# Optimization experiments

Hardware: AMD Instinct MI355X
Metric: run time of the kernel (lower is better)

Reference implementation:

```python
import jax, jax.numpy as jnp
import numpy as np
import math

B, T, H, W = 32, 256, 16, 16
NE, NH, NL = 768, 12, 8
DH = NE // NH
SEQ_LEN = 1024


def _ln(x, g, b, eps=1e-5):
    m = jnp.mean(x, axis=-1, keepdims=True)
    v = jnp.mean((x - m) ** 2, axis=-1, keepdims=True)
    return (x - m) * jax.lax.rsqrt(v + eps) * g + b


def setup_inputs() -> dict:
    key = jax.random.key(0)
    ks = jax.random.split(key, 24)
    s = 0.02
    d = {}
    d["img_feat"] = jax.random.normal(ks[0], (B, 2048, H, W), jnp.float32)
    d["vm_patches"] = jax.random.normal(ks[1], (B, T, 256), jnp.float32)
    d["fm_patches"] = jax.random.normal(ks[2], (B, T, 256), jnp.float32)
    # token embedding params
    d["conv_w"] = jax.random.normal(ks[3], (NE // 2, 2048, 3, 3), jnp.float32) * s
    d["conv_b"] = jnp.zeros((NE // 2,), jnp.float32)
    d["vm_w"] = jax.random.normal(ks[4], (256, NE // 4), jnp.float32) * s
    d["vm_b"] = jnp.zeros((NE // 4,), jnp.float32)
    d["fm_w"] = jax.random.normal(ks[5], (256, NE // 4), jnp.float32) * s
    d["fm_b"] = jnp.zeros((NE // 4,), jnp.float32)
    d["pos_emb"] = jax.random.normal(ks[6], (SEQ_LEN, NE), jnp.float32) * s
    # stacked per-layer block params (leading dim NL, consumed by lax.scan)
    d["ln1_g"] = jnp.ones((NL, NE), jnp.float32)
    d["ln1_b"] = jnp.zeros((NL, NE), jnp.float32)
    d["Wq"] = jax.random.normal(ks[7], (NL, NE, NE), jnp.float32) * s
    d["bq"] = jnp.zeros((NL, NE), jnp.float32)
    d["Wk"] = jax.random.normal(ks[8], (NL, NE, NE), jnp.float32) * s
    d["bk"] = jnp.zeros((NL, NE), jnp.float32)
    d["Wv"] = jax.random.normal(ks[9], (NL, NE, NE), jnp.float32) * s
    d["bv"] = jnp.zeros((NL, NE), jnp.float32)
    d["Wo"] = jax.random.normal(ks[10], (NL, NE, NE), jnp.float32) * s
    d["bo"] = jnp.zeros((NL, NE), jnp.float32)
    d["ln2_g"] = jnp.ones((NL, NE), jnp.float32)
    d["ln2_b"] = jnp.zeros((NL, NE), jnp.float32)
    d["W1"] = jax.random.normal(ks[11], (NL, NE, 4 * NE), jnp.float32) * s
    d["b1"] = jnp.zeros((NL, 4 * NE), jnp.float32)
    d["W2"] = jax.random.normal(ks[12], (NL, 4 * NE, NE), jnp.float32) * s
    d["b2"] = jnp.zeros((NL, NE), jnp.float32)
    # prediction head params
    d["dec_ln1_g"] = jnp.ones((NE,), jnp.float32)
    d["dec_ln1_b"] = jnp.zeros((NE,), jnp.float32)
    d["dec_w"] = jax.random.normal(ks[13], (NE, NE), jnp.float32) * s
    d["dec_b"] = jnp.zeros((NE,), jnp.float32)
    d["dec_ln2_g"] = jnp.ones((NE,), jnp.float32)
    d["dec_ln2_b"] = jnp.zeros((NE,), jnp.float32)
    d["head_w"] = jax.random.normal(ks[14], (NE, 256), jnp.float32) * s
    d["head_b"] = jnp.zeros((256,), jnp.float32)
    return d


def reference(img_feat, vm_patches, fm_patches, conv_w, conv_b, vm_w, vm_b, fm_w, fm_b,
              pos_emb, ln1_g, ln1_b, Wq, bq, Wk, bk, Wv, bv, Wo, bo, ln2_g, ln2_b,
              W1, b1, W2, b2, dec_ln1_g, dec_ln1_b, dec_w, dec_b, dec_ln2_g, dec_ln2_b,
              head_w, head_b):
    # conv token embed: [B,2048,H,W] -> [B, NE//2, H, W] -> [B, T, NE//2]
    i_emb = jax.lax.conv_general_dilated(
        img_feat, conv_w, (1, 1), "SAME",
        dimension_numbers=("NCHW", "OIHW", "NCHW")) + conv_b[None, :, None, None]
    i_emb = i_emb.reshape(B, NE // 2, T).transpose(0, 2, 1)
    vm_emb = vm_patches @ vm_w + vm_b  # [B,T,NE//4]
    fm_emb = fm_patches @ fm_w + fm_b  # [B,T,NE//4]
    x = jnp.concatenate([i_emb, vm_emb, fm_emb], axis=2) + pos_emb[:T][None]  # [B,T,NE]

    scale = 1.0 / math.sqrt(DH)

    def block(x, p):
        g1, bb1_, wq, bq_, wk, bk_, wv, bv_, wo, bo_, g2, bb2_, w1, bm1, w2, bm2 = p
        h = _ln(x, g1, bb1_)
        q = (h @ wq + bq_).reshape(B, T, NH, DH)
        k = (h @ wk + bk_).reshape(B, T, NH, DH)
        v = (h @ wv + bv_).reshape(B, T, NH, DH)
        # mask in the original forward is hard-coded all-ones -> no masking
        att = jax.nn.softmax(jnp.einsum('bthd,bshd->bhts', q, k) * scale, axis=-1)
        y = jnp.einsum('bhts,bshd->bthd', att, v).reshape(B, T, NE)
        x = x + y @ wo + bo_
        h2 = _ln(x, g2, bb2_)
        x = x + jax.nn.gelu(h2 @ w1 + bm1, approximate=False) @ w2 + bm2
        return x, None

    x, _ = jax.lax.scan(block, x, (ln1_g, ln1_b, Wq, bq, Wk, bk, Wv, bv, Wo, bo,
                                   ln2_g, ln2_b, W1, b1, W2, b2))

    # Transformer_Prediction head
    x = _ln(x, dec_ln1_g, dec_ln1_b)
    x = jax.nn.gelu(x @ dec_w + dec_b, approximate=False)
    x = _ln(x, dec_ln2_g, dec_ln2_b)
    return x @ head_w + head_b  # [B,T,256]
```

## Files before the change

### kernel.cpp

```cpp
#include <hip/hip_runtime.h>
#include <stdint.h>

typedef short short8 __attribute__((ext_vector_type(8)));
typedef float v4f __attribute__((ext_vector_type(4)));

#define EPI_BF16    0
#define EPI_GELU    1
#define EPI_XPOS    3
#define EPI_ATOM    5
#define EPI_ATOMOUT 6

__device__ __forceinline__ uint16_t f2bf(float f) {
  uint32_t u = __float_as_uint(f);
  u += 0x7fffu + ((u >> 16) & 1u);
  return (uint16_t)(u >> 16);
}
__device__ __forceinline__ float bf2f(uint16_t h) {
  return __uint_as_float(((uint32_t)h) << 16);
}
__device__ __forceinline__ float gelu_f(float v) {
  return 0.5f * v * (1.f + erff(v * 0.70710678118654752f));
}
__device__ __forceinline__ void gld16(const uint16_t* g, uint16_t* l) {
  __builtin_amdgcn_global_load_lds(
      (const __attribute__((address_space(1))) void*)g,
      (__attribute__((address_space(3))) void*)l, 16, 0, 0);
}

struct TDesc {
  const float* src;
  uint16_t* dst;
  int K, N, batch;
  long long sstride, dstride;
  int tilesK, tilesN;
  long long tileStart;
};
struct TTable {
  TDesc d[12];
  int nd;
  long long totalTiles;
};

__global__ __launch_bounds__(256) void transpose_convert_kernel(TTable tt) {
  __shared__ float tile[32][33];
  const int tid = threadIdx.x;
  for (long long t = blockIdx.x; t < tt.totalTiles; t += gridDim.x) {
    int di = 0;
    while (di + 1 < tt.nd && t >= tt.d[di + 1].tileStart) di++;
    const TDesc d = tt.d[di];
    long long loc = t - d.tileStart;
    int perB = d.tilesK * d.tilesN;
    int bi = (int)(loc / perB);
    int r = (int)(loc % perB);
    int tk = r / d.tilesN, tn = r % d.tilesN;
    const float* src = d.src + (long long)bi * d.sstride;
    uint16_t* dst = d.dst + (long long)bi * d.dstride;
    int k0 = tk * 32, n0 = tn * 32;
#pragma unroll
    for (int p = 0; p < 4; p++) {
      int i = (tid >> 5) + p * 8;
      int k = k0 + i, n = n0 + (tid & 31);
      float v = 0.f;
      if (k < d.K && n < d.N) v = src[(long long)k * d.N + n];
      tile[i][tid & 31] = v;
    }
    __syncthreads();
#pragma unroll
    for (int p = 0; p < 4; p++) {
      int i = (tid >> 5) + p * 8;
      int n = n0 + i, k = k0 + (tid & 31);
      if (n < d.N && k < d.K) dst[(long long)n * d.K + k] = f2bf(tile[tid & 31][i]);
    }
    __syncthreads();
  }
}

__global__ __launch_bounds__(256) void conv_w_transpose(const float* __restrict__ src,
                                                        uint16_t* __restrict__ dst) {
  __shared__ float lds[2304];
  const int n = blockIdx.y;
  const int c0 = blockIdx.x * 256;
  const float* s = src + (size_t)n * 18432 + (size_t)c0 * 9;
  for (int j = threadIdx.x; j < 2304; j += 256) lds[j] = s[j];
  __syncthreads();
#pragma unroll
  for (int tap = 0; tap < 9; tap++)
    dst[(size_t)n * 18432 + tap * 2048 + c0 + threadIdx.x] =
        f2bf(lds[threadIdx.x * 9 + tap]);
}

__global__ __launch_bounds__(256) void img_pad_kernel(const float* __restrict__ img,
                                                      uint16_t* __restrict__ imgp) {
  __shared__ float tile[64][65];
  const int tid = threadIdx.x;
  const int b = blockIdx.z, ict = blockIdx.y, xyt = blockIdx.x;
  const int ic0 = ict * 64, xy0 = xyt * 64;
  const float* src = img + ((size_t)b * 2048 + ic0) * 256 + xy0;
#pragma unroll
  for (int p = 0; p < 16; p++) {
    int i = (tid >> 6) + p * 4;
    int j = tid & 63;
    tile[i][j] = src[(size_t)i * 256 + j];
  }
  __syncthreads();
#pragma unroll
  for (int p = 0; p < 16; p++) {
    int j = (tid >> 6) + p * 4;
    int i = tid & 63;
    int xy = xy0 + j;
    int y = xy >> 4, x = xy & 15;
    imgp[(((size_t)b * 18 + y + 1) * 18 + (x + 1)) * 2048 + ic0 + i] = f2bf(tile[i][j]);
  }
}

__global__ __launch_bounds__(256) void prep_kernel(const float* __restrict__ bq,
                                                   const float* __restrict__ bk,
                                                   const float* __restrict__ bv,
                                                   float* __restrict__ bqkv,
                                                   const float* __restrict__ vm,
                                                   const float* __restrict__ fm,
                                                   uint16_t* __restrict__ vmb,
                                                   uint16_t* __restrict__ fmb) {
  int idx = blockIdx.x * 256 + threadIdx.x;
  if (idx < 2097152) {
    vmb[idx] = f2bf(vm[idx]);
    fmb[idx] = f2bf(fm[idx]);
  }
  if (idx < 18432) {
    int l = idx / 2304, c = idx % 2304;
    float v = (c < 768) ? bq[l * 768 + c]
                        : ((c < 1536) ? bk[l * 768 + c - 768] : bv[l * 768 + c - 1536]);
    bqkv[idx] = v;
  }
}

__global__ __launch_bounds__(256) void xinit_kernel(const float* __restrict__ convb,
                                                    const float* __restrict__ pos,
                                                    float* __restrict__ x) {
  int idx = blockIdx.x * 256 + threadIdx.x;
  if (idx >= 8192 * 384) return;
  int m = idx / 384, n = idx % 384;
  x[(size_t)m * 768 + n] = convb[n] + pos[(size_t)(m & 255) * 768 + n];
}

template <int BF16IN>
__global__ __launch_bounds__(256) void ln_kernel(const void* __restrict__ inv,
                                                 const float* __restrict__ g,
                                                 const float* __restrict__ bta,
                                                 uint16_t* __restrict__ out) {
  const int row = blockIdx.x;
  const int tid = threadIdx.x;
  const float* inf = (const float*)inv;
  const uint16_t* inb = (const uint16_t*)inv;
  const size_t base = (size_t)row * 768;
  float v[3];
#pragma unroll
  for (int i = 0; i < 3; i++) {
    int c = tid + i * 256;
    v[i] = BF16IN ? bf2f(inb[base + c]) : inf[base + c];
  }
  float s = v[0] + v[1] + v[2];
  float s2 = v[0] * v[0] + v[1] * v[1] + v[2] * v[2];
#pragma unroll
  for (int d = 1; d < 64; d <<= 1) {
    s += __shfl_xor(s, d, 64);
    s2 += __shfl_xor(s2, d, 64);
  }
  __shared__ float ps[4], ps2[4];
  int wave = tid >> 6, lane = tid & 63;
  if (lane == 0) { ps[wave] = s; ps2[wave] = s2; }
  __syncthreads();
  s = ps[0] + ps[1] + ps[2] + ps[3];
  s2 = ps2[0] + ps2[1] + ps2[2] + ps2[3];
  float mean = s * (1.f / 768.f);
  float var = s2 * (1.f / 768.f) - mean * mean;
  float rs = rsqrtf(var + 1e-5f);
#pragma unroll
  for (int i = 0; i < 3; i++) {
    int c = tid + i * 256;
    out[base + c] = f2bf((v[i] - mean) * rs * g[c] + bta[c]);
  }
}

template <int AMODE, int EPI>
__global__ __launch_bounds__(256, 4) void gemm_kernel(
    const uint16_t* __restrict__ A, const uint16_t* __restrict__ Bt,
    const float* __restrict__ bias, int N, int K,
    float* xout,
    const float* __restrict__ pos, int colOff,
    uint16_t* __restrict__ outb, float* __restrict__ outf, int ldc) {
  __shared__ uint16_t ldsA[8192];
  __shared__ uint16_t ldsB[4096];
  const int tid = threadIdx.x;
  const int lane = tid & 63, wave = tid >> 6;
  const int l15 = lane & 15, q8 = (lane >> 4) << 3;
  const int row0 = blockIdx.x * 128, col0 = blockIdx.y * 64;
  const int kPer = K / (int)gridDim.z;
  const int kbeg = kPer * (int)blockIdx.z;
  const int wm = wave & 1, wn = wave >> 1;

  const uint16_t* srcP[6];
  uint16_t* dstP[6];
  bool isA[6];
#pragma unroll
  for (int c = 0; c < 6; c++) {
    int j = wave * 6 + c;
    if (j < 16) {
      int mt8 = j >> 1, ks = j & 1;
      int m = row0 + mt8 * 16 + l15;
      const uint16_t* s;
      if (AMODE == 0) {
        s = A + (size_t)m * K + ks * 32 + q8;
      } else {
        int b_ = m >> 8, y_ = (m >> 4) & 15, x_ = m & 15;
        s = A + ((size_t)((b_ * 18 + y_) * 18 + x_)) * 2048 + ks * 32 + q8;
      }
      srcP[c] = s;
      dstP[c] = &ldsA[j * 512];
      isA[c] = true;
    } else {
      int fb = j - 16;
      int nt = fb >> 1, ks = fb & 1;
      int n = col0 + nt * 16 + l15;
      srcP[c] = Bt + (size_t)n * K + ks * 32 + q8;
      dstP[c] = &ldsB[fb * 512];
      isA[c] = false;
    }
  }

  v4f acc[4][2];
#pragma unroll
  for (int i = 0; i < 4; i++)
#pragma unroll
    for (int j = 0; j < 2; j++) acc[i][j] = (v4f){0.f, 0.f, 0.f, 0.f};

  for (int k0 = kbeg; k0 < kbeg + kPer; k0 += 64) {
    size_t ao;
    if (AMODE == 1) {
      int kq = k0 >> 11;
      int ky = (kq >= 6) ? 2 : ((kq >= 3) ? 1 : 0);
      int kx = kq - ky * 3;
      ao = (size_t)((ky * 18 + kx) * 2048) + (size_t)(k0 & 2047);
    } else {
      ao = (size_t)k0;
    }
    __syncthreads();
#pragma unroll
    for (int c = 0; c < 6; c++) {
      size_t offs = (AMODE == 1) ? (isA[c] ? ao : (size_t)k0) : (size_t)k0;
      gld16(srcP[c] + offs, dstP[c]);
    }
    __syncthreads();
#pragma unroll
    for (int ks = 0; ks < 2; ks++) {
      short8 af[4], bfr[2];
#pragma unroll
      for (int mt = 0; mt < 4; mt++)
        af[mt] = *(const short8*)&ldsA[(((wm * 4 + mt) * 2) + ks) * 512 + lane * 8];
#pragma unroll
      for (int nt = 0; nt < 2; nt++)
        bfr[nt] = *(const short8*)&ldsB[(((wn * 2 + nt) * 2) + ks) * 512 + lane * 8];
#pragma unroll
      for (int mt = 0; mt < 4; mt++)
#pragma unroll
        for (int nt = 0; nt < 2; nt++)
          acc[mt][nt] =
              __builtin_amdgcn_mfma_f32_16x16x32_bf16(af[mt], bfr[nt], acc[mt][nt], 0, 0, 0);
    }
  }

#pragma unroll
  for (int mt = 0; mt < 4; mt++) {
    int mbase = row0 + wm * 64 + mt * 16 + ((lane >> 4) << 2);
#pragma unroll
    for (int nt = 0; nt < 2; nt++) {
      int n = col0 + wn * 32 + nt * 16 + l15;
      float bv;
      if (EPI == EPI_ATOM)
        bv = (bias != nullptr && blockIdx.z == 0) ? bias[n] : 0.f;
      else if (EPI == EPI_ATOMOUT)
        bv = (blockIdx.z == 0) ? bias[n] : 0.f;
      else
        bv = bias[n];
      v4f a = acc[mt][nt];
#pragma unroll
      for (int r = 0; r < 4; r++) {
        int m = mbase + r;
        float v = a[r] + bv;
        if (EPI == EPI_BF16) {
          outb[(size_t)m * ldc + n] = f2bf(v);
        } else if (EPI == EPI_GELU) {
          outb[(size_t)m * ldc + n] = f2bf(gelu_f(v));
        } else if (EPI == EPI_XPOS) {
          xout[(size_t)m * 768 + colOff + n] = v + pos[(size_t)(m & 255) * 768 + colOff + n];
        } else if (EPI == EPI_ATOM) {
          atomicAdd(&xout[(size_t)m * 768 + colOff + n], v);
        } else if (EPI == EPI_ATOMOUT) {
          atomicAdd(&outf[(size_t)m * ldc + n], v);
        }
      }
    }
  }
}

template <int AMODE, int EPI>
__global__ __launch_bounds__(256, 2) void gemm128_kernel(
    const uint16_t* __restrict__ A, const uint16_t* __restrict__ Bt,
    const float* __restrict__ bias, int N, int K,
    float* xout,
    const float* __restrict__ pos, int colOff,
    uint16_t* __restrict__ outb, float* __restrict__ outf, int ldc) {
  __shared__ uint16_t lds[2][16384];
  const int tid = threadIdx.x;
  const int lane = tid & 63, wave = tid >> 6;
  const int l15 = lane & 15, q8 = (lane >> 4) << 3;
  const int row0 = blockIdx.x * 128, col0 = blockIdx.y * 128;
  const int kPer = K / (int)gridDim.z;
  const int kbeg = kPer * (int)blockIdx.z;
  const int nt = kPer >> 6;
  const int wm = wave & 1, wn = wave >> 1;

  const uint16_t* srcP[8];
  int off[8];
  bool isAv[8];
#pragma unroll
  for (int c = 0; c < 8; c++) {
    int j = wave * 8 + c;
    if (j < 16) {
      int mt8 = j >> 1, ks = j & 1;
      int m = row0 + mt8 * 16 + l15;
      const uint16_t* s;
      if (AMODE == 0) {
        s = A + (size_t)m * K + ks * 32 + q8;
      } else {
        int b_ = m >> 8, y_ = (m >> 4) & 15, x_ = m & 15;
        s = A + ((size_t)((b_ * 18 + y_) * 18 + x_)) * 2048 + ks * 32 + q8;
      }
      srcP[c] = s;
      off[c] = j * 512;
      isAv[c] = true;
    } else {
      int fb = j - 16;
      int nt16 = fb >> 1, ks = fb & 1;
      int n = col0 + nt16 * 16 + l15;
      srcP[c] = Bt + (size_t)n * K + ks * 32 + q8;
      off[c] = 8192 + fb * 512;
      isAv[c] = false;
    }
  }

  auto STAGE = [&](int t) {
    int k0 = kbeg + t * 64;
    size_t aoB = (size_t)k0, aoA;
    if (AMODE == 1) {
      int kq = k0 >> 11;
      int ky = (kq >= 6) ? 2 : ((kq >= 3) ? 1 : 0);
      int kx = kq - ky * 3;
      aoA = (size_t)((ky * 18 + kx) * 2048) + (size_t)(k0 & 2047);
    } else {
      aoA = aoB;
    }
    uint16_t* lb = &lds[t & 1][0];
#pragma unroll
    for (int c = 0; c < 8; c++) gld16(srcP[c] + (isAv[c] ? aoA : aoB), lb + off[c]);
  };

  v4f acc[4][4];
#pragma unroll
  for (int i = 0; i < 4; i++)
#pragma unroll
    for (int j = 0; j < 4; j++) acc[i][j] = (v4f){0.f, 0.f, 0.f, 0.f};

  STAGE(0);
  if (nt > 1) STAGE(1);

  for (int t = 0; t < nt; t++) {
    if (t + 1 < nt)
      asm volatile("s_waitcnt vmcnt(8)" ::: "memory");
    else
      asm volatile("s_waitcnt vmcnt(0)" ::: "memory");
    __builtin_amdgcn_s_barrier();

    const uint16_t* lb = &lds[t & 1][0];
#pragma unroll
    for (int ks = 0; ks < 2; ks++) {
      short8 af[4], bfr[4];
#pragma unroll
      for (int mt = 0; mt < 4; mt++)
        af[mt] = *(const short8*)&lb[(((wm * 4 + mt) * 2) + ks) * 512 + lane * 8];
#pragma unroll
      for (int nt2 = 0; nt2 < 4; nt2++)
        bfr[nt2] = *(const short8*)&lb[8192 + (((wn * 4 + nt2) * 2) + ks) * 512 + lane * 8];
#pragma unroll
      for (int mt = 0; mt < 4; mt++)
#pragma unroll
        for (int nt2 = 0; nt2 < 4; nt2++)
          acc[mt][nt2] =
              __builtin_amdgcn_mfma_f32_16x16x32_bf16(af[mt], bfr[nt2], acc[mt][nt2], 0, 0, 0);
    }

    __builtin_amdgcn_s_barrier();
    if (t + 2 < nt) STAGE(t + 2);
  }

#pragma unroll
  for (int mt = 0; mt < 4; mt++) {
    int mbase = row0 + wm * 64 + mt * 16 + ((lane >> 4) << 2);
#pragma unroll
    for (int nt2 = 0; nt2 < 4; nt2++) {
      int n = col0 + wn * 64 + nt2 * 16 + l15;
      float bv;
      if (EPI == EPI_ATOM)
        bv = (bias != nullptr && blockIdx.z == 0) ? bias[n] : 0.f;
      else if (EPI == EPI_ATOMOUT)
        bv = (blockIdx.z == 0) ? bias[n] : 0.f;
      else
        bv = bias[n];
      v4f a = acc[mt][nt2];
#pragma unroll
      for (int r = 0; r < 4; r++) {
        int m = mbase + r;
        float v = a[r] + bv;
        if (EPI == EPI_BF16) {
          outb[(size_t)m * ldc + n] = f2bf(v);
        } else if (EPI == EPI_GELU) {
          outb[(size_t)m * ldc + n] = f2bf(gelu_f(v));
        } else if (EPI == EPI_XPOS) {
          xout[(size_t)m * 768 + colOff + n] = v + pos[(size_t)(m & 255) * 768 + colOff + n];
        } else if (EPI == EPI_ATOM) {
          atomicAdd(&xout[(size_t)m * 768 + colOff + n], v);
        } else if (EPI == EPI_ATOMOUT) {
          atomicAdd(&outf[(size_t)m * ldc + n], v);
        }
      }
    }
  }
}

__global__ __launch_bounds__(256) void attn_kernel(const uint16_t* __restrict__ qkv,
                                                   uint16_t* __restrict__ y) {
  __shared__ uint16_t KP[18432];
  __shared__ uint16_t Vt[64 * 264];
  uint16_t* Kl = KP;
  uint16_t(*Pl)[16 * 264] = (uint16_t(*)[16 * 264])KP;
  const int tid = threadIdx.x, lane = tid & 63, wave = tid >> 6;
  const int qc = blockIdx.x, h = blockIdx.y, b = blockIdx.z;
  const uint16_t* base = qkv + (size_t)b * 256 * 2304;
  const uint16_t* kb = base + 768 + h * 64;
  const uint16_t* vb = base + 1536 + h * 64;

#pragma unroll
  for (int i = 0; i < 8; i++) {
    int c = i * 256 + tid;
    int t = c >> 3, dh = (c & 7) * 8;
    uint4 d = *(const uint4*)(kb + (size_t)t * 2304 + dh);
    *(uint4*)&Kl[t * 72 + dh] = d;
  }
#pragma unroll
  for (int i = 0; i < 8; i++) {
    int c = i * 256 + tid;
    int t = c >> 3, dh = (c & 7) * 8;
    uint4 d = *(const uint4*)(vb + (size_t)t * 2304 + dh);
    const uint16_t* e = (const uint16_t*)&d;
#pragma unroll
    for (int j = 0; j < 8; j++) Vt[(dh + j) * 264 + t] = e[j];
  }
  __syncthreads();

  const int t0 = qc * 64 + wave * 16;
  const uint16_t* qb = base + h * 64;
  const int l15 = lane & 15, q4 = (lane >> 4) << 3;
  short8 aq0 = *(const short8*)(qb + (size_t)(t0 + l15) * 2304 + q4);
  short8 aq1 = *(const short8*)(qb + (size_t)(t0 + l15) * 2304 + 32 + q4);

  v4f s[16];
#pragma unroll
  for (int jt = 0; jt < 16; jt++) {
    short8 b0 = *(const short8*)&Kl[(jt * 16 + l15) * 72 + q4];
    short8 b1 = *(const short8*)&Kl[(jt * 16 + l15) * 72 + 32 + q4];
    v4f z = (v4f){0.f, 0.f, 0.f, 0.f};
    z = __builtin_amdgcn_mfma_f32_16x16x32_bf16(aq0, b0, z, 0, 0, 0);
    s[jt] = __builtin_amdgcn_mfma_f32_16x16x32_bf16(aq1, b1, z, 0, 0, 0);
  }

  float mx[4], sm[4];
#pragma unroll
  for (int r = 0; r < 4; r++) mx[r] = -1e30f;
#pragma unroll
  for (int jt = 0; jt < 16; jt++)
#pragma unroll
    for (int r = 0; r < 4; r++) {
      float v = s[jt][r] * 0.125f;
      s[jt][r] = v;
      mx[r] = fmaxf(mx[r], v);
    }
#pragma unroll
  for (int r = 0; r < 4; r++) {
#pragma unroll
    for (int d = 1; d < 16; d <<= 1) mx[r] = fmaxf(mx[r], __shfl_xor(mx[r], d, 64));
    sm[r] = 0.f;
  }
#pragma unroll
  for (int jt = 0; jt < 16; jt++)
#pragma unroll
    for (int r = 0; r < 4; r++) {
      float e = __expf(s[jt][r] - mx[r]);
      s[jt][r] = e;
      sm[r] += e;
    }
#pragma unroll
  for (int r = 0; r < 4; r++) {
#pragma unroll
    for (int d = 1; d < 16; d <<= 1) sm[r] += __shfl_xor(sm[r], d, 64);
    sm[r] = 1.f / sm[r];
  }

  __syncthreads();

  const int rbase = (lane >> 4) << 2;
#pragma unroll
  for (int jt = 0; jt < 16; jt++)
#pragma unroll
    for (int r = 0; r < 4; r++)
      Pl[wave][(rbase + r) * 264 + jt * 16 + l15] = f2bf(s[jt][r] * sm[r]);
  __syncthreads();

  v4f o[4];
#pragma unroll
  for (int nt = 0; nt < 4; nt++) o[nt] = (v4f){0.f, 0.f, 0.f, 0.f};
#pragma unroll
  for (int ks = 0; ks < 8; ks++) {
    short8 ap = *(const short8*)&Pl[wave][l15 * 264 + ks * 32 + q4];
#pragma unroll
    for (int nt = 0; nt < 4; nt++) {
      short8 bv8 = *(const short8*)&Vt[(nt * 16 + l15) * 264 + ks * 32 + q4];
      o[nt] = __builtin_amdgcn_mfma_f32_16x16x32_bf16(ap, bv8, o[nt], 0, 0, 0);
    }
  }
#pragma unroll
  for (int nt = 0; nt < 4; nt++)
#pragma unroll
    for (int r = 0; r < 4; r++)
      y[(size_t)(b * 256 + t0 + rbase + r) * 768 + h * 64 + nt * 16 + l15] = f2bf(o[nt][r]);
}

extern "C" void kernel_launch(void* const* d_in, const int* in_sizes, int n_in,
                              void* d_out, int out_size, void* d_ws, size_t ws_size,
                              hipStream_t stream) {
  const float* img   = (const float*)d_in[0];
  const float* vmp   = (const float*)d_in[1];
  const float* fmp   = (const float*)d_in[2];
  const float* convw = (const float*)d_in[3];
  const float* convb = (const float*)d_in[4];
  const float* vmw   = (const float*)d_in[5];
  const float* vmb_  = (const float*)d_in[6];
  const float* fmw   = (const float*)d_in[7];
  const float* fmb_  = (const float*)d_in[8];
  const float* pos   = (const float*)d_in[9];
  const float* ln1g  = (const float*)d_in[10];
  const float* ln1b  = (const float*)d_in[11];
  const float* Wq    = (const float*)d_in[12];
  const float* bq    = (const float*)d_in[13];
  const float* Wk    = (const float*)d_in[14];
  const float* bk    = (const float*)d_in[15];
  const float* Wv    = (const float*)d_in[16];
  const float* bv    = (const float*)d_in[17];
  const float* Wo    = (const float*)d_in[18];
  const float* bo    = (const float*)d_in[19];
  const float* ln2g  = (const float*)d_in[20];
  const float* ln2b  = (const float*)d_in[21];
  const float* W1    = (const float*)d_in[22];
  const float* b1    = (const float*)d_in[23];
  const float* W2    = (const float*)d_in[24];
  const float* b2    = (const float*)d_in[25];
  const float* dln1g = (const float*)d_in[26];
  const float* dln1b = (const float*)d_in[27];
  const float* decw  = (const float*)d_in[28];
  const float* decb  = (const float*)d_in[29];
  const float* dln2g = (const float*)d_in[30];
  const float* dln2b = (const float*)d_in[31];
  const float* headw = (const float*)d_in[32];
  const float* headb = (const float*)d_in[33];
  float* out = (float*)d_out;

  char* wsb = (char*)d_ws;
  size_t off = 0;
  auto alloc = [&](size_t nbytes) -> void* {
    off = (off + 255) & ~(size_t)255;
    void* p = wsb + off;
    off += nbytes;
    return p;
  };
  uint16_t* WtQKV  = (uint16_t*)alloc(8ull * 2304 * 768 * 2);
  uint16_t* WtO    = (uint16_t*)alloc(8ull * 768 * 768 * 2);
  uint16_t* Wt1    = (uint16_t*)alloc(8ull * 3072 * 768 * 2);
  uint16_t* Wt2    = (uint16_t*)alloc(8ull * 768 * 3072 * 2);
  uint16_t* WtConv = (uint16_t*)alloc(384ull * 9 * 2048 * 2);
  uint16_t* WtVm   = (uint16_t*)alloc(192ull * 256 * 2);
  uint16_t* WtFm   = (uint16_t*)alloc(192ull * 256 * 2);
  uint16_t* WtDec  = (uint16_t*)alloc(768ull * 768 * 2);
  uint16_t* WtHead = (uint16_t*)alloc(256ull * 768 * 2);
  uint16_t* imgp   = (uint16_t*)alloc(32ull * 18 * 18 * 2048 * 2);
  uint16_t* vmb    = (uint16_t*)alloc(8192ull * 256 * 2);
  uint16_t* fmb    = (uint16_t*)alloc(8192ull * 256 * 2);
  float*    bqkv   = (float*)alloc(8ull * 2304 * 4);
  float*    x      = (float*)alloc(8192ull * 768 * 4);
  uint16_t* hbuf   = (uint16_t*)alloc(8192ull * 768 * 2);
  uint16_t* qkvb   = (uint16_t*)alloc(8192ull * 2304 * 2);
  uint16_t* ybuf   = (uint16_t*)alloc(8192ull * 768 * 2);
  uint16_t* ubuf   = (uint16_t*)alloc(8192ull * 3072 * 2);
  uint16_t* u2buf  = (uint16_t*)alloc(8192ull * 768 * 2);
  if (off > ws_size) return;

  hipMemsetAsync(imgp, 0, 32ull * 18 * 18 * 2048 * 2, stream);
  hipMemsetAsync(out, 0, (size_t)out_size * 4, stream);

  TTable tt;
  int nd = 0;
  long long tiles = 0;
  auto addT = [&](const float* src, uint16_t* dst, int K, int N, int batch,
                  long long sstr, long long dstr) {
    TDesc& d = tt.d[nd];
    d.src = src; d.dst = dst; d.K = K; d.N = N; d.batch = batch;
    d.sstride = sstr; d.dstride = dstr;
    d.tilesK = (K + 31) / 32; d.tilesN = (N + 31) / 32;
    d.tileStart = tiles;
    tiles += (long long)d.tilesK * d.tilesN * batch;
    nd++;
  };
  addT(Wq, WtQKV,           768, 768, 8, 589824, 1769472);
  addT(Wk, WtQKV + 589824,  768, 768, 8, 589824, 1769472);
  addT(Wv, WtQKV + 1179648, 768, 768, 8, 589824, 1769472);
  addT(Wo, WtO,             768, 768, 8, 589824, 589824);
  addT(W1, Wt1,             768, 3072, 8, 2359296, 2359296);
  addT(W2, Wt2,             3072, 768, 8, 2359296, 2359296);
  addT(vmw, WtVm,           256, 192, 1, 0, 0);
  addT(fmw, WtFm,           256, 192, 1, 0, 0);
  addT(decw, WtDec,         768, 768, 1, 0, 0);
  addT(headw, WtHead,       768, 256, 1, 0, 0);
  tt.nd = nd;
  tt.totalTiles = tiles;

  transpose_convert_kernel<<<(int)tiles, 256, 0, stream>>>(tt);
  conv_w_transpose<<<dim3(8, 384), 256, 0, stream>>>(convw, WtConv);
  img_pad_kernel<<<dim3(4, 32, 32), 256, 0, stream>>>(img, imgp);
  prep_kernel<<<8192, 256, 0, stream>>>(bq, bk, bv, bqkv, vmp, fmp, vmb, fmb);
  xinit_kernel<<<12288, 256, 0, stream>>>(convb, pos, x);

  gemm128_kernel<1, EPI_ATOM><<<dim3(64, 3, 4), 256, 0, stream>>>(
      imgp, WtConv, nullptr, 384, 18432, x, nullptr, 0, nullptr, nullptr, 0);
  gemm_kernel<0, EPI_XPOS><<<dim3(64, 3), 256, 0, stream>>>(
      vmb, WtVm, vmb_, 192, 256, x, pos, 384, nullptr, nullptr, 0);
  gemm_kernel<0, EPI_XPOS><<<dim3(64, 3), 256, 0, stream>>>(
      fmb, WtFm, fmb_, 192, 256, x, pos, 576, nullptr, nullptr, 0);

  for (int l = 0; l < 8; l++) {
    ln_kernel<0><<<8192, 256, 0, stream>>>(x, ln1g + l * 768, ln1b + l * 768, hbuf);
    gemm128_kernel<0, EPI_BF16><<<dim3(64, 18), 256, 0, stream>>>(
        hbuf, WtQKV + (size_t)l * 1769472, bqkv + l * 2304, 2304, 768,
        nullptr, nullptr, 0, qkvb, nullptr, 2304);
    attn_kernel<<<dim3(4, 12, 32), 256, 0, stream>>>(qkvb, ybuf);
    gemm128_kernel<0, EPI_ATOM><<<dim3(64, 6, 2), 256, 0, stream>>>(
        ybuf, WtO + (size_t)l * 589824, bo + l * 768, 768, 768,
        x, nullptr, 0, nullptr, nullptr, 0);
    ln_kernel<0><<<8192, 256, 0, stream>>>(x, ln2g + l * 768, ln2b + l * 768, hbuf);
    gemm128_kernel<0, EPI_GELU><<<dim3(64, 24), 256, 0, stream>>>(
        hbuf, Wt1 + (size_t)l * 2359296, b1 + l * 3072, 3072, 768,
        nullptr, nullptr, 0, ubuf, nullptr, 3072);
    gemm128_kernel<0, EPI_ATOM><<<dim3(64, 6, 2), 256, 0, stream>>>(
        ubuf, Wt2 + (size_t)l * 2359296, b2 + l * 768, 768, 3072,
        x, nullptr, 0, nullptr, nullptr, 0);
  }

  ln_kernel<0><<<8192, 256, 0, stream>>>(x, dln1g, dln1b, hbuf);
  gemm128_kernel<0, EPI_GELU><<<dim3(64, 6), 256, 0, stream>>>(
      hbuf, WtDec, decb, 768, 768, nullptr, nullptr, 0, u2buf, nullptr, 768);
  ln_kernel<1><<<8192, 256, 0, stream>>>(u2buf, dln2g, dln2b, hbuf);
  gemm128_kernel<0, EPI_ATOMOUT><<<dim3(64, 2, 2), 256, 0, stream>>>(
      hbuf, WtHead, headb, 256, 768, nullptr, nullptr, 0, nullptr, out, 256);
}
```

Measured before the change: 3.521 ms.

## Add 256x256-tile 8-wave GEMM kernel with phased ping-pong loads for main GEMMs

Introduces a 512-thread GEMM kernel that computes 256x256 output tiles using 128KB of dynamic LDS, double buffered. The K loop is split into four MFMA quarter-phases interleaved with staged global-to-LDS loads, using barriers and s_setprio. The conv, QKV, O-proj and MLP GEMMs move to it; conv weights are padded to 512 columns and zeroed. This aims for more data reuse per loaded byte and better load/compute overlap, at the cost of fewer blocks per GPU, wasted padded conv columns, and higher register pressure.

Result: faster. 3.390 ms (-3.7%).

```diff
diff --git a/kernel.cpp b/kernel.cpp
--- a/kernel.cpp
+++ b/kernel.cpp
@@ -201,30 +201,20 @@
 
   const uint16_t* srcP[6];
   uint16_t* dstP[6];
-  bool isA[6];
 #pragma unroll
   for (int c = 0; c < 6; c++) {
     int j = wave * 6 + c;
     if (j < 16) {
       int mt8 = j >> 1, ks = j & 1;
       int m = row0 + mt8 * 16 + l15;
-      const uint16_t* s;
-      if (AMODE == 0) {
-        s = A + (size_t)m * K + ks * 32 + q8;
-      } else {
-        int b_ = m >> 8, y_ = (m >> 4) & 15, x_ = m & 15;
-        s = A + ((size_t)((b_ * 18 + y_) * 18 + x_)) * 2048 + ks * 32 + q8;
-      }
-      srcP[c] = s;
+      srcP[c] = A + (size_t)m * K + ks * 32 + q8;
       dstP[c] = &ldsA[j * 512];
-      isA[c] = true;
     } else {
       int fb = j - 16;
       int nt = fb >> 1, ks = fb & 1;
       int n = col0 + nt * 16 + l15;
       srcP[c] = Bt + (size_t)n * K + ks * 32 + q8;
       dstP[c] = &ldsB[fb * 512];
-      isA[c] = false;
     }
   }
 
@@ -235,21 +225,9 @@
     for (int j = 0; j < 2; j++) acc[i][j] = (v4f){0.f, 0.f, 0.f, 0.f};
 
   for (int k0 = kbeg; k0 < kbeg + kPer; k0 += 64) {
-    size_t ao;
-    if (AMODE == 1) {
-      int kq = k0 >> 11;
-      int ky = (kq >= 6) ? 2 : ((kq >= 3) ? 1 : 0);
-      int kx = kq - ky * 3;
-      ao = (size_t)((ky * 18 + kx) * 2048) + (size_t)(k0 & 2047);
-    } else {
-      ao = (size_t)k0;
-    }
     __syncthreads();
 #pragma unroll
-    for (int c = 0; c < 6; c++) {
-      size_t offs = (AMODE == 1) ? (isA[c] ? ao : (size_t)k0) : (size_t)k0;
-      gld16(srcP[c] + offs, dstP[c]);
-    }
+    for (int c = 0; c < 6; c++) gld16(srcP[c] + (size_t)k0, dstP[c]);
     __syncthreads();
 #pragma unroll
     for (int ks = 0; ks < 2; ks++) {
@@ -303,12 +281,11 @@
   }
 }
 
-template <int AMODE, int EPI>
+template <int EPI>
 __global__ __launch_bounds__(256, 2) void gemm128_kernel(
     const uint16_t* __restrict__ A, const uint16_t* __restrict__ Bt,
     const float* __restrict__ bias, int N, int K,
     float* xout,
-    const float* __restrict__ pos, int colOff,
     uint16_t* __restrict__ outb, float* __restrict__ outf, int ldc) {
   __shared__ uint16_t lds[2][16384];
   const int tid = threadIdx.x;
@@ -322,47 +299,28 @@
 
   const uint16_t* srcP[8];
   int off[8];
-  bool isAv[8];
 #pragma unroll
   for (int c = 0; c < 8; c++) {
     int j = wave * 8 + c;
     if (j < 16) {
       int mt8 = j >> 1, ks = j & 1;
       int m = row0 + mt8 * 16 + l15;
-      const uint16_t* s;
-      if (AMODE == 0) {
-        s = A + (size_t)m * K + ks * 32 + q8;
-      } else {
-        int b_ = m >> 8, y_ = (m >> 4) & 15, x_ = m & 15;
-        s = A + ((size_t)((b_ * 18 + y_) * 18 + x_)) * 2048 + ks * 32 + q8;
-      }
-      srcP[c] = s;
+      srcP[c] = A + (size_t)m * K + kbeg + ks * 32 + q8;
       off[c] = j * 512;
-      isAv[c] = true;
     } else {
       int fb = j - 16;
       int nt16 = fb >> 1, ks = fb & 1;
       int n = col0 + nt16 * 16 + l15;
-      srcP[c] = Bt + (size_t)n * K + ks * 32 + q8;
+      srcP[c] = Bt + (size_t)n * K + kbeg + ks * 32 + q8;
       off[c] = 8192 + fb * 512;
-      isAv[c] = false;
     }
   }
 
   auto STAGE = [&](int t) {
-    int k0 = kbeg + t * 64;
-    size_t aoB = (size_t)k0, aoA;
-    if (AMODE == 1) {
-      int kq = k0 >> 11;
-      int ky = (kq >= 6) ? 2 : ((kq >= 3) ? 1 : 0);
-      int kx = kq - ky * 3;
-      aoA = (size_t)((ky * 18 + kx) * 2048) + (size_t)(k0 & 2047);
-    } else {
-      aoA = aoB;
-    }
+    size_t ko = (size_t)(t * 64);
     uint16_t* lb = &lds[t & 1][0];
 #pragma unroll
-    for (int c = 0; c < 8; c++) gld16(srcP[c] + (isAv[c] ? aoA : aoB), lb + off[c]);
+    for (int c = 0; c < 8; c++) gld16(srcP[c] + ko, lb + off[c]);
   };
 
   v4f acc[4][4];
@@ -410,9 +368,7 @@
     for (int nt2 = 0; nt2 < 4; nt2++) {
       int n = col0 + wn * 64 + nt2 * 16 + l15;
       float bv;
-      if (EPI == EPI_ATOM)
-        bv = (bias != nullptr && blockIdx.z == 0) ? bias[n] : 0.f;
-      else if (EPI == EPI_ATOMOUT)
+      if (EPI == EPI_ATOMOUT)
         bv = (blockIdx.z == 0) ? bias[n] : 0.f;
       else
         bv = bias[n];
@@ -425,12 +381,200 @@
           outb[(size_t)m * ldc + n] = f2bf(v);
         } else if (EPI == EPI_GELU) {
           outb[(size_t)m * ldc + n] = f2bf(gelu_f(v));
-        } else if (EPI == EPI_XPOS) {
-          xout[(size_t)m * 768 + colOff + n] = v + pos[(size_t)(m & 255) * 768 + colOff + n];
-        } else if (EPI == EPI_ATOM) {
-          atomicAdd(&xout[(size_t)m * 768 + colOff + n], v);
         } else if (EPI == EPI_ATOMOUT) {
           atomicAdd(&outf[(size_t)m * ldc + n], v);
+        }
+      }
+    }
+  }
+}
+
+template <int AMODE, int EPI>
+__global__ __launch_bounds__(512, 2) void gemm256_kernel(
+    const uint16_t* __restrict__ A, const uint16_t* __restrict__ Bt,
+    const float* __restrict__ bias, int N, int K,
+    float* xout, uint16_t* __restrict__ outb, float* __restrict__ outf, int ldc) {
+  extern __shared__ uint16_t lds[];
+  const int tid = threadIdx.x;
+  const int lane = tid & 63, wave = tid >> 6;
+  const int l15 = lane & 15, q8 = (lane >> 4) << 3;
+  const int row0 = blockIdx.x * 256, col0 = blockIdx.y * 256;
+  const int kPer = K / (int)gridDim.z;
+  const int kbeg = kPer * (int)blockIdx.z;
+  const int nt = kPer >> 6;
+  const int wm = wave >> 2, wn = wave & 3;
+
+  const uint16_t* src[4][2];
+  int ldsoff[4][2];
+#pragma unroll
+  for (int c = 0; c < 2; c++) {
+    int sub = wave * 2 + c;
+    int hf = sub >> 1, ks = sub & 1;
+    int kin = ks * 32 + q8;
+    int m0 = row0 + hf * 16 + l15;
+    int m1 = m0 + 128;
+    if (AMODE == 0) {
+      src[0][c] = A + (size_t)m0 * K + kin;
+      src[3][c] = A + (size_t)m1 * K + kin;
+    } else {
+      int b0_ = m0 >> 8, y0_ = (m0 >> 4) & 15, x0_ = m0 & 15;
+      src[0][c] = A + ((size_t)((b0_ * 18 + y0_) * 18 + x0_)) * 2048 + kin;
+      int b1_ = m1 >> 8, y1_ = (m1 >> 4) & 15, x1_ = m1 & 15;
+      src[3][c] = A + ((size_t)((b1_ * 18 + y1_) * 18 + x1_)) * 2048 + kin;
+    }
+    src[1][c] = Bt + (size_t)(col0 + hf * 16 + l15) * K + kin;
+    src[2][c] = Bt + (size_t)(col0 + 128 + hf * 16 + l15) * K + kin;
+    ldsoff[0][c] = sub * 512;
+    ldsoff[3][c] = (16 + sub) * 512;
+    ldsoff[1][c] = 16384 + sub * 512;
+    ldsoff[2][c] = 16384 + (16 + sub) * 512;
+  }
+
+#define STAGEH(TT, Q)                                                          \
+  do {                                                                         \
+    int t_ = (TT);                                                             \
+    if (t_ < nt) {                                                             \
+      int k0_ = kbeg + t_ * 64;                                                \
+      size_t o_;                                                               \
+      if (AMODE == 1 && ((Q) == 0 || (Q) == 3)) {                              \
+        int kq_ = k0_ >> 11;                                                   \
+        int ky_ = (kq_ >= 6) ? 2 : ((kq_ >= 3) ? 1 : 0);                       \
+        int kx_ = kq_ - ky_ * 3;                                               \
+        o_ = (size_t)((ky_ * 18 + kx_) * 2048) + (size_t)(k0_ & 2047);         \
+      } else {                                                                 \
+        o_ = (size_t)k0_;                                                      \
+      }                                                                        \
+      uint16_t* lb_ = &lds[(t_ & 1) * 32768];                                  \
+      gld16(src[Q][0] + o_, lb_ + ldsoff[Q][0]);                               \
+      gld16(src[Q][1] + o_, lb_ + ldsoff[Q][1]);                               \
+    }                                                                          \
+  } while (0)
+
+  v4f acc[8][4];
+#pragma unroll
+  for (int i = 0; i < 8; i++)
+#pragma unroll
+    for (int j = 0; j < 4; j++) acc[i][j] = (v4f){0.f, 0.f, 0.f, 0.f};
+
+  STAGEH(0, 0); STAGEH(0, 1); STAGEH(0, 2); STAGEH(0, 3);
+  STAGEH(1, 1); STAGEH(1, 0);
+  asm volatile("s_waitcnt vmcnt(4)" ::: "memory");
+  __builtin_amdgcn_s_barrier();
+
+  short8 a_[4][2], b0_[2][2], b1_[2][2];
+
+  for (int t = 0; t < nt; t++) {
+    const int bufo = (t & 1) * 32768;
+
+#pragma unroll
+    for (int mt = 0; mt < 4; mt++)
+#pragma unroll
+      for (int ks = 0; ks < 2; ks++)
+        a_[mt][ks] = *(const short8*)&lds[bufo + ((wm * 8 + mt) * 2 + ks) * 512 + lane * 8];
+#pragma unroll
+    for (int nl = 0; nl < 2; nl++)
+#pragma unroll
+      for (int ks = 0; ks < 2; ks++)
+        b0_[nl][ks] =
+            *(const short8*)&lds[bufo + 16384 + ((wn * 4 + nl) * 2 + ks) * 512 + lane * 8];
+    STAGEH(t + 1, 2);
+    __builtin_amdgcn_s_barrier();
+    __builtin_amdgcn_s_setprio(1);
+#pragma unroll
+    for (int mt = 0; mt < 4; mt++)
+#pragma unroll
+      for (int nl = 0; nl < 2; nl++)
+#pragma unroll
+        for (int ks = 0; ks < 2; ks++)
+          acc[mt][nl] =
+              __builtin_amdgcn_mfma_f32_16x16x32_bf16(a_[mt][ks], b0_[nl][ks], acc[mt][nl], 0, 0, 0);
+    __builtin_amdgcn_s_setprio(0);
+    __builtin_amdgcn_s_barrier();
+
+#pragma unroll
+    for (int nl = 0; nl < 2; nl++)
+#pragma unroll
+      for (int ks = 0; ks < 2; ks++)
+        b1_[nl][ks] =
+            *(const short8*)&lds[bufo + 16384 + ((wn * 4 + 2 + nl) * 2 + ks) * 512 + lane * 8];
+    STAGEH(t + 1, 3);
+    __builtin_amdgcn_s_barrier();
+    __builtin_amdgcn_s_setprio(1);
+#pragma unroll
+    for (int mt = 0; mt < 4; mt++)
+#pragma unroll
+      for (int nl = 0; nl < 2; nl++)
+#pragma unroll
+        for (int ks = 0; ks < 2; ks++)
+          acc[mt][2 + nl] =
+              __builtin_amdgcn_mfma_f32_16x16x32_bf16(a_[mt][ks], b1_[nl][ks], acc[mt][2 + nl], 0, 0, 0);
+    __builtin_amdgcn_s_setprio(0);
+    __builtin_amdgcn_s_barrier();
+
+#pragma unroll
+    for (int mt = 0; mt < 4; mt++)
+#pragma unroll
+      for (int ks = 0; ks < 2; ks++)
+        a_[mt][ks] =
+            *(const short8*)&lds[bufo + ((wm * 8 + 4 + mt) * 2 + ks) * 512 + lane * 8];
+    STAGEH(t + 2, 1);
+    __builtin_amdgcn_s_barrier();
+    __builtin_amdgcn_s_setprio(1);
+#pragma unroll
+    for (int mt = 0; mt < 4; mt++)
+#pragma unroll
+      for (int nl = 0; nl < 2; nl++)
+#pragma unroll
+        for (int ks = 0; ks < 2; ks++)
+          acc[4 + mt][2 + nl] =
+              __builtin_amdgcn_mfma_f32_16x16x32_bf16(a_[mt][ks], b1_[nl][ks], acc[4 + mt][2 + nl], 0, 0, 0);
+    __builtin_amdgcn_s_setprio(0);
+    __builtin_amdgcn_s_barrier();
+
+    STAGEH(t + 2, 0);
+    if (t < nt - 1) {
+      if (t == nt - 2)
+        asm volatile("s_waitcnt vmcnt(0)" ::: "memory");
+      else
+        asm volatile("s_waitcnt vmcnt(4)" ::: "memory");
+    }
+    __builtin_amdgcn_s_barrier();
+    __builtin_amdgcn_s_setprio(1);
+#pragma unroll
+    for (int mt = 0; mt < 4; mt++)
+#pragma unroll
+      for (int nl = 0; nl < 2; nl++)
+#pragma unroll
+        for (int ks = 0; ks < 2; ks++)
+          acc[4 + mt][nl] =
+              __builtin_amdgcn_mfma_f32_16x16x32_bf16(a_[mt][ks], b0_[nl][ks], acc[4 + mt][nl], 0, 0, 0);
+    __builtin_amdgcn_s_setprio(0);
+    __builtin_amdgcn_s_barrier();
+  }
+#undef STAGEH
+
+#pragma unroll
+  for (int mt = 0; mt < 8; mt++) {
+    int mbase = row0 + wm * 128 + mt * 16 + ((lane >> 4) << 2);
+#pragma unroll
+    for (int nl = 0; nl < 4; nl++) {
+      int n = col0 + wn * 64 + nl * 16 + l15;
+      float bv;
+      if (EPI == EPI_ATOM)
+        bv = (bias != nullptr && blockIdx.z == 0) ? bias[n] : 0.f;
+      else
+        bv = bias[n];
+      v4f a = acc[mt][nl];
+#pragma unroll
+      for (int r = 0; r < 4; r++) {
+        int m = mbase + r;
+        float v = a[r] + bv;
+        if (EPI == EPI_BF16) {
+          outb[(size_t)m * ldc + n] = f2bf(v);
+        } else if (EPI == EPI_GELU) {
+          outb[(size_t)m * ldc + n] = f2bf(gelu_f(v));
+        } else if (EPI == EPI_ATOM) {
+          atomicAdd(&xout[(size_t)m * 768 + n], v);
         }
       }
     }
@@ -595,7 +739,7 @@
   uint16_t* WtO    = (uint16_t*)alloc(8ull * 768 * 768 * 2);
   uint16_t* Wt1    = (uint16_t*)alloc(8ull * 3072 * 768 * 2);
   uint16_t* Wt2    = (uint16_t*)alloc(8ull * 768 * 3072 * 2);
-  uint16_t* WtConv = (uint16_t*)alloc(384ull * 9 * 2048 * 2);
+  uint16_t* WtConv = (uint16_t*)alloc(512ull * 9 * 2048 * 2);
   uint16_t* WtVm   = (uint16_t*)alloc(192ull * 256 * 2);
   uint16_t* WtFm   = (uint16_t*)alloc(192ull * 256 * 2);
   uint16_t* WtDec  = (uint16_t*)alloc(768ull * 768 * 2);
@@ -613,7 +757,17 @@
   if (off > ws_size) return;
 
   hipMemsetAsync(imgp, 0, 32ull * 18 * 18 * 2048 * 2, stream);
+  hipMemsetAsync(WtConv, 0, 512ull * 9 * 2048 * 2, stream);
   hipMemsetAsync(out, 0, (size_t)out_size * 4, stream);
+
+  hipFuncSetAttribute((const void*)gemm256_kernel<1, EPI_ATOM>,
+                      hipFuncAttributeMaxDynamicSharedMemorySize, 131072);
+  hipFuncSetAttribute((const void*)gemm256_kernel<0, EPI_ATOM>,
+                      hipFuncAttributeMaxDynamicSharedMemorySize, 131072);
+  hipFuncSetAttribute((const void*)gemm256_kernel<0, EPI_BF16>,
+                      hipFuncAttributeMaxDynamicSharedMemorySize, 131072);
+  hipFuncSetAttribute((const void*)gemm256_kernel<0, EPI_GELU>,
+                      hipFuncAttributeMaxDynamicSharedMemorySize, 131072);
 
   TTable tt;
   int nd = 0;
@@ -647,8 +801,8 @@
   prep_kernel<<<8192, 256, 0, stream>>>(bq, bk, bv, bqkv, vmp, fmp, vmb, fmb);
   xinit_kernel<<<12288, 256, 0, stream>>>(convb, pos, x);
 
-  gemm128_kernel<1, EPI_ATOM><<<dim3(64, 3, 4), 256, 0, stream>>>(
-      imgp, WtConv, nullptr, 384, 18432, x, nullptr, 0, nullptr, nullptr, 0);
+  gemm256_kernel<1, EPI_ATOM><<<dim3(32, 2, 4), 512, 131072, stream>>>(
+      imgp, WtConv, nullptr, 512, 18432, x, nullptr, nullptr, 0);
   gemm_kernel<0, EPI_XPOS><<<dim3(64, 3), 256, 0, stream>>>(
       vmb, WtVm, vmb_, 192, 256, x, pos, 384, nullptr, nullptr, 0);
   gemm_kernel<0, EPI_XPOS><<<dim3(64, 3), 256, 0, stream>>>(
@@ -656,26 +810,26 @@
 
   for (int l = 0; l < 8; l++) {
     ln_kernel<0><<<8192, 256, 0, stream>>>(x, ln1g + l * 768, ln1b + l * 768, hbuf);
-    gemm128_kernel<0, EPI_BF16><<<dim3(64, 18), 256, 0, stream>>>(
+    gemm256_kernel<0, EPI_BF16><<<dim3(32, 9), 512, 131072, stream>>>(
         hbuf, WtQKV + (size_t)l * 1769472, bqkv + l * 2304, 2304, 768,
-        nullptr, nullptr, 0, qkvb, nullptr, 2304);
+        nullptr, qkvb, nullptr, 2304);
     attn_kernel<<<dim3(4, 12, 32), 256, 0, stream>>>(qkvb, ybuf);
-    gemm128_kernel<0, EPI_ATOM><<<dim3(64, 6, 2), 256, 0, stream>>>(
+    gemm256_kernel<0, EPI_ATOM><<<dim3(32, 3, 2), 512, 131072, stream>>>(
         ybuf, WtO + (size_t)l * 589824, bo + l * 768, 768, 768,
-        x, nullptr, 0, nullptr, nullptr, 0);
+        x, nullptr, nullptr, 0);
     ln_kernel<0><<<8192, 256, 0, stream>>>(x, ln2g + l * 768, ln2b + l * 768, hbuf);
-    gemm128_kernel<0, EPI_GELU><<<dim3(64, 24), 256, 0, stream>>>(
+    gemm256_kernel<0, EPI_GELU><<<dim3(32, 12), 512, 131072, stream>>>(
         hbuf, Wt1 + (size_t)l * 2359296, b1 + l * 3072, 3072, 768,
-        nullptr, nullptr, 0, ubuf, nullptr, 3072);
-    gemm128_kernel<0, EPI_ATOM><<<dim3(64, 6, 2), 256, 0, stream>>>(
+        nullptr, ubuf, nullptr, 3072);
+    gemm256_kernel<0, EPI_ATOM><<<dim3(32, 3, 2), 512, 131072, stream>>>(
         ubuf, Wt2 + (size_t)l * 2359296, b2 + l * 768, 768, 3072,
-        x, nullptr, 0, nullptr, nullptr, 0);
+        x, nullptr, nullptr, 0);
   }
 
   ln_kernel<0><<<8192, 256, 0, stream>>>(x, dln1g, dln1b, hbuf);
-  gemm128_kernel<0, EPI_GELU><<<dim3(64, 6), 256, 0, stream>>>(
-      hbuf, WtDec, decb, 768, 768, nullptr, nullptr, 0, u2buf, nullptr, 768);
+  gemm128_kernel<EPI_GELU><<<dim3(64, 6), 256, 0, stream>>>(
+      hbuf, WtDec, decb, 768, 768, nullptr, u2buf, nullptr, 768);
   ln_kernel<1><<<8192, 256, 0, stream>>>(u2buf, dln2g, dln2b, hbuf);
-  gemm128_kernel<0, EPI_ATOMOUT><<<dim3(64, 2, 2), 256, 0, stream>>>(
-      hbuf, WtHead, headb, 256, 768, nullptr, nullptr, 0, nullptr, out, 256);
-}
+  gemm128_kernel<EPI_ATOMOUT><<<dim3(64, 2, 2), 256, 0, stream>>>(
+      hbuf, WtHead, headb, 256, 768, nullptr, nullptr, out, 256);
+}
```
